# Performance work log

Measured on AMD Instinct MI355X. Metric: run time of the kernel, lower is better.

## Reference

```python
import jax, jax.numpy as jnp
import numpy as np

B, T, C, H = 2, 2048, 1024, 16
HD = C // H  # head_size = 64
EPS = 1e-5


def setup_inputs() -> dict:
    key = jax.random.key(0)
    ks = jax.random.split(key, 12)
    s = lambda fan_in: 1.0 / np.sqrt(fan_in)
    return {
        "x": jax.random.normal(ks[0], (B, T, C), jnp.float32),
        # attention projections, stored [in, out] so y = x @ W
        "Wq": jax.random.normal(ks[1], (C, C), jnp.float32) * s(C),
        "Wk": jax.random.normal(ks[2], (C, C), jnp.float32) * s(C),
        "Wv": jax.random.normal(ks[3], (C, C), jnp.float32) * s(C),
        "Wo": jax.random.normal(ks[4], (C, C), jnp.float32) * s(C),
        "bo": jnp.zeros((C,), jnp.float32),
        "ln1_g": jnp.ones((C,), jnp.float32),
        "ln1_b": jnp.zeros((C,), jnp.float32),
        "ln2_g": jnp.ones((C,), jnp.float32),
        "ln2_b": jnp.zeros((C,), jnp.float32),
        "W1": jax.random.normal(ks[5], (C, 4 * C), jnp.float32) * s(C),
        "b1": jnp.zeros((4 * C,), jnp.float32),
        "W2": jax.random.normal(ks[6], (4 * C, C), jnp.float32) * s(4 * C),
        "b2": jnp.zeros((C,), jnp.float32),
    }


def _layernorm(x, g, b):
    mu = jnp.mean(x, axis=-1, keepdims=True)
    var = jnp.mean(jnp.square(x - mu), axis=-1, keepdims=True)
    return (x - mu) * jax.lax.rsqrt(var + EPS) * g + b


def reference(x, Wq, Wk, Wv, Wo, bo, ln1_g, ln1_b, ln2_g, ln2_b, W1, b1, W2, b2):
    # Dropout layers are inference no-ops (eval mode).
    Bz, Tz, Cz = x.shape
    h = _layernorm(x, ln1_g, ln1_b)
    # fused multi-head projections (equivalent to per-head Linears concatenated)
    q = (h @ Wq).reshape(Bz, Tz, H, HD)
    k = (h @ Wk).reshape(Bz, Tz, H, HD)
    v = (h @ Wv).reshape(Bz, Tz, H, HD)
    scores = jnp.einsum("bqhd,bkhd->bhqk", q, k) / np.sqrt(HD).astype(np.float32)
    causal = jnp.tril(jnp.ones((Tz, Tz), bool))
    scores = jnp.where(causal, scores, -jnp.inf)
    attn = jax.nn.softmax(scores, axis=-1)
    out = jnp.einsum("bhqk,bkhd->bqhd", attn, v).reshape(Bz, Tz, Cz)
    x = x + out @ Wo + bo
    h2 = _layernorm(x, ln2_g, ln2_b)
    ff = jax.nn.relu(h2 @ W1 + b1) @ W2 + b2
    return x + ff
```

## Files before the change

### kernel.cpp

```cpp
#include <hip/hip_runtime.h>
#include <hip/hip_bf16.h>
#include <stdint.h>

#define B_  2
#define T_  2048
#define C_  1024
#define H_  16
#define HD_ 64
#define M_  4096
#define FF_ 4096

typedef unsigned short ushort_t;
typedef __bf16 bf16x8 __attribute__((ext_vector_type(8)));
typedef float  f32x4  __attribute__((ext_vector_type(4)));
typedef float  f32x16 __attribute__((ext_vector_type(16)));
typedef unsigned int u32x2 __attribute__((ext_vector_type(2)));
typedef unsigned int u32x4 __attribute__((ext_vector_type(4)));

#define C2_ 0.1803368801111204f

__device__ inline ushort_t f2bf(float f) {
  uint32_t u = __builtin_bit_cast(uint32_t, f);
  u += 0x7fffu + ((u >> 16) & 1u);
  return (ushort_t)(u >> 16);
}
__device__ inline uint32_t pk2(float lo, float hi) {
  return (uint32_t)f2bf(lo) | ((uint32_t)f2bf(hi) << 16);
}

__device__ inline void gload_lds16(const void* g, void* l) {
  __builtin_amdgcn_global_load_lds(
      (const __attribute__((address_space(1))) uint32_t*)g,
      (__attribute__((address_space(3))) uint32_t*)l, 16, 0, 0);
}

__device__ inline int qswz(int row, int byte_in_row) {
  return row * 128 + (byte_in_row ^ ((row & 7) << 4));
}

__global__ __launch_bounds__(256) void lnorm_kernel(
    const float* __restrict__ x, const float* __restrict__ g,
    const float* __restrict__ b, ushort_t* __restrict__ o) {
  int row = blockIdx.x;
  int tid = threadIdx.x;
  const float4* xr = (const float4*)(x + (size_t)row * C_);
  float4 xv = xr[tid];
  float s  = xv.x + xv.y + xv.z + xv.w;
  float s2 = xv.x*xv.x + xv.y*xv.y + xv.z*xv.z + xv.w*xv.w;
#pragma unroll
  for (int off = 32; off; off >>= 1) {
    s  += __shfl_down(s,  off);
    s2 += __shfl_down(s2, off);
  }
  __shared__ float rs[4], rq[4];
  int wid = tid >> 6;
  if ((tid & 63) == 0) { rs[wid] = s; rq[wid] = s2; }
  __syncthreads();
  float tot  = rs[0] + rs[1] + rs[2] + rs[3];
  float tot2 = rq[0] + rq[1] + rq[2] + rq[3];
  float mu   = tot * (1.0f / C_);
  float var  = tot2 * (1.0f / C_) - mu * mu;
  float rstd = rsqrtf(var + 1e-5f);
  float4 gv = ((const float4*)g)[tid];
  float4 bv = ((const float4*)b)[tid];
  float y0 = (xv.x - mu) * rstd * gv.x + bv.x;
  float y1 = (xv.y - mu) * rstd * gv.y + bv.y;
  float y2 = (xv.z - mu) * rstd * gv.z + bv.z;
  float y3 = (xv.w - mu) * rstd * gv.w + bv.w;
  uint2 pk;
  pk.x = (uint32_t)f2bf(y0) | ((uint32_t)f2bf(y1) << 16);
  pk.y = (uint32_t)f2bf(y2) | ((uint32_t)f2bf(y3) << 16);
  *(uint2*)(o + (size_t)row * C_ + tid * 4) = pk;
}

__global__ __launch_bounds__(256) void tcast_kernel(
    const float* __restrict__ W, ushort_t* __restrict__ Wt, int K, int N) {
  __shared__ float t[32][33];
  int bn = blockIdx.x, bk = blockIdx.y;
  int tx = threadIdx.x & 31, ty = threadIdx.x >> 5;
#pragma unroll
  for (int i = 0; i < 4; ++i)
    t[ty + i*8][tx] = W[(size_t)(bk*32 + ty + i*8) * N + bn*32 + tx];
  __syncthreads();
#pragma unroll
  for (int i = 0; i < 4; ++i)
    Wt[(size_t)(bn*32 + ty + i*8) * K + bk*32 + tx] = f2bf(t[tx][ty + i*8]);
}

__global__ __launch_bounds__(256) void vtrans_kernel(
    const ushort_t* __restrict__ qkv, ushort_t* __restrict__ vt) {
  __shared__ ushort_t t[32][33];
  int tt = blockIdx.x;
  int cc = blockIdx.y;
  int bb = blockIdx.z;
  int tx = threadIdx.x & 31, ty = threadIdx.x >> 5;
#pragma unroll
  for (int i = 0; i < 4; ++i)
    t[ty + i*8][tx] = qkv[(size_t)(bb*T_ + tt*32 + ty + i*8)*3072 + 2048 + cc*32 + tx];
  __syncthreads();
  int crow = threadIdx.x >> 4;
  int ucol = threadIdx.x & 15;
#pragma unroll
  for (int i = 0; i < 2; ++i) {
    int c = crow + i*16;
    uint32_t vlo = t[ucol*2][c], vhi = t[ucol*2 + 1][c];
    *(uint32_t*)&vt[(size_t)(bb*1024 + cc*32 + c)*T_ + tt*32 + ucol*2] =
        vlo | (vhi << 16);
  }
}

template<int BN, int BIAS, int RELU, int RESID, int OUTBF16>
__global__ __launch_bounds__(256) void gemm_kernel(
    const ushort_t* __restrict__ A, const ushort_t* __restrict__ Bt,
    const float* __restrict__ bias, const float* __restrict__ resid,
    void* __restrict__ outp, int M, int N, int K) {
  constexpr int NFR = BN / 32;
  __shared__ __align__(16) ushort_t As[2][128*32];
  __shared__ __align__(16) ushort_t Bs[2][BN*32];
  int bn = blockIdx.x, bm = blockIdx.y;
  int tid = threadIdx.x;
  int lane = tid & 63, wid = tid >> 6;
  int wr = (wid >> 1) * 64, wc = (wid & 1) * (BN / 2);
  int r = lane & 15, g = lane >> 4;
  int srow = tid >> 2, scc = (tid & 3) * 8;
  f32x4 acc[4][NFR] = {};
  int nk = K >> 5;

  const ushort_t* Abase = A  + (size_t)(bm*128) * K;
  const ushort_t* Bbase = Bt + (size_t)(bn*BN) * K;

#define STAGE_(bi, kt_)                                                        \
  do {                                                                         \
    gload_lds16(Abase + (size_t)srow * K + (kt_)*32 + scc, &As[bi][tid*8]);    \
    gload_lds16(Abase + (size_t)(srow + 64) * K + (kt_)*32 + scc,              \
                &As[bi][(tid + 256)*8]);                                       \
    gload_lds16(Bbase + (size_t)srow * K + (kt_)*32 + scc, &Bs[bi][tid*8]);    \
    if (BN == 128)                                                             \
      gload_lds16(Bbase + (size_t)(srow + 64) * K + (kt_)*32 + scc,            \
                  &Bs[bi][(tid + 256)*8]);                                     \
  } while (0)

  STAGE_(0, 0);
  __syncthreads();
  int buf = 0;
  for (int kt = 0; kt < nk; ++kt) {
    if (kt + 1 < nk) STAGE_(buf ^ 1, kt + 1);
    bf16x8 af[4], bfv[NFR];
#pragma unroll
    for (int m = 0; m < 4; ++m)
      af[m] = *(const bf16x8*)&As[buf][(wr + m*16 + r)*32 + g*8];
#pragma unroll
    for (int n = 0; n < NFR; ++n)
      bfv[n] = *(const bf16x8*)&Bs[buf][(wc + n*16 + r)*32 + g*8];
#pragma unroll
    for (int m = 0; m < 4; ++m)
#pragma unroll
      for (int n = 0; n < NFR; ++n)
        acc[m][n] = __builtin_amdgcn_mfma_f32_16x16x32_bf16(
            af[m], bfv[n], acc[m][n], 0, 0, 0);
    __syncthreads();
    buf ^= 1;
  }
#undef STAGE_

#pragma unroll
  for (int m = 0; m < 4; ++m)
#pragma unroll
    for (int n = 0; n < NFR; ++n)
#pragma unroll
      for (int e = 0; e < 4; ++e) {
        int row = bm*128 + wr + m*16 + g*4 + e;
        int col = bn*BN + wc + n*16 + r;
        float v = acc[m][n][e];
        if (BIAS)  v += bias[col];
        if (RESID) v += resid[(size_t)row * N + col];
        if (RELU)  v = fmaxf(v, 0.0f);
        if (OUTBF16) ((ushort_t*)outp)[(size_t)row * N + col] = f2bf(v);
        else         ((float*)outp)[(size_t)row * N + col]    = v;
      }
}

__global__ __launch_bounds__(256) void attn_kernel(
    const ushort_t* __restrict__ q, const ushort_t* __restrict__ k,
    const ushort_t* __restrict__ vt, ushort_t* __restrict__ o, int ldq) {
  int bid = blockIdx.x;
  int qbb = 15 - (bid & 15);
  int hh = (bid >> 4) & 15;
  int bb = bid >> 8;
  __shared__ __align__(16) ushort_t Ks[64*64];
  __shared__ __align__(16) ushort_t Vts[64*64];
  int tid = threadIdx.x, lane = tid & 63, w = tid >> 6;
  int qi = lane & 31, hi = lane >> 5;
  int qrow0 = qbb*128 + w*32;
  int qg = qrow0 + qi;
  int lt = 2*qbb + (w >> 1);
  int nkv = 2*qbb + 2;

  const ushort_t* qbase = q + ((size_t)(bb*T_ + qg))*ldq + hh*64;
  bf16x8 qv[4];
#pragma unroll
  for (int c = 0; c < 4; ++c)
    qv[c] = *(const bf16x8*)(qbase + c*16 + hi*8);

  const ushort_t* kbase = k  + ((size_t)bb*T_)*ldq + hh*64;
  const ushort_t* vbase = vt + ((size_t)(bb*1024 + hh*64))*T_;

  int r0s = tid >> 3;
  int s0  = ((tid & 7) ^ (r0s & 7)) * 8;

  f32x16 O0 = {}, O1 = {};
  float mrun = -1e30f, lrun = 0.f;

  for (int kt = 0; kt < nkv; ++kt) {
    gload_lds16(kbase + ((size_t)(kt*64 + r0s))*ldq + s0,      &Ks[tid*8]);
    gload_lds16(kbase + ((size_t)(kt*64 + r0s + 32))*ldq + s0, &Ks[(tid+256)*8]);
    gload_lds16(vbase + (size_t)r0s*T_ + kt*64 + s0,           &Vts[tid*8]);
    gload_lds16(vbase + (size_t)(r0s+32)*T_ + kt*64 + s0,      &Vts[(tid+256)*8]);
    __syncthreads();
    if (kt <= lt) {
      f32x16 a0 = {}, a1 = {};
#pragma unroll
      for (int c = 0; c < 4; ++c) {
        bf16x8 k0 = *(const bf16x8*)((char*)Ks + qswz(qi,      c*32 + hi*16));
        bf16x8 k1 = *(const bf16x8*)((char*)Ks + qswz(32 + qi, c*32 + hi*16));
        a0 = __builtin_amdgcn_mfma_f32_32x32x16_bf16(k0, qv[c], a0, 0, 0, 0);
        a1 = __builtin_amdgcn_mfma_f32_32x32x16_bf16(k1, qv[c], a1, 0, 0, 0);
      }
      if (kt == lt) {
        int kof = kt*64 + 4*hi;
#pragma unroll
        for (int rg = 0; rg < 16; ++rg) {
          int kp = kof + (rg & 3) + 8*(rg >> 2);
          if (kp > qg)      a0[rg] = -1e30f;
          if (kp + 32 > qg) a1[rg] = -1e30f;
        }
      }
      float tm = -1e30f;
#pragma unroll
      for (int rg = 0; rg < 16; ++rg) tm = fmaxf(tm, fmaxf(a0[rg], a1[rg]));
      tm = fmaxf(tm, __shfl_xor(tm, 32));
      float mnew = fmaxf(mrun, tm);
      float sf = exp2f((mrun - mnew) * C2_);
      mrun = mnew;
      float mc = mnew * C2_;
#pragma unroll
      for (int rg = 0; rg < 16; ++rg) {
        a0[rg] = exp2f(a0[rg]*C2_ - mc);
        a1[rg] = exp2f(a1[rg]*C2_ - mc);
      }
      float rs = 0.f;
#pragma unroll
      for (int rg = 0; rg < 16; ++rg) rs += a0[rg] + a1[rg];
      rs += __shfl_xor(rs, 32);
      lrun = lrun*sf + rs;
#pragma unroll
      for (int rg = 0; rg < 16; ++rg) { O0[rg] *= sf; O1[rg] *= sf; }
      bf16x8 pf[4];
#pragma unroll
      for (int kb = 0; kb < 2; ++kb)
#pragma unroll
        for (int jj = 0; jj < 2; ++jj) {
          int rb = jj*8;
          float v0 = kb ? a1[rb+0] : a0[rb+0], v1 = kb ? a1[rb+1] : a0[rb+1];
          float v2 = kb ? a1[rb+2] : a0[rb+2], v3 = kb ? a1[rb+3] : a0[rb+3];
          float v4 = kb ? a1[rb+4] : a0[rb+4], v5 = kb ? a1[rb+5] : a0[rb+5];
          float v6 = kb ? a1[rb+6] : a0[rb+6], v7 = kb ? a1[rb+7] : a0[rb+7];
          uint32_t d0 = pk2(v0, v1), d1 = pk2(v2, v3);
          uint32_t e0 = pk2(v4, v5), e1 = pk2(v6, v7);
          uint32_t pd0 = __shfl_xor(d0, 32), pd1 = __shfl_xor(d1, 32);
          uint32_t pe0 = __shfl_xor(e0, 32), pe1 = __shfl_xor(e1, 32);
          u32x4 fw;
          fw[0] = hi ? pe0 : d0;
          fw[1] = hi ? pe1 : d1;
          fw[2] = hi ? e0  : pd0;
          fw[3] = hi ? e1  : pd1;
          pf[kb*2 + jj] = __builtin_bit_cast(bf16x8, fw);
        }
#pragma unroll
      for (int kk = 0; kk < 4; ++kk) {
        bf16x8 vv0 = *(const bf16x8*)((char*)Vts + qswz(qi,      kk*32 + hi*16));
        bf16x8 vv1 = *(const bf16x8*)((char*)Vts + qswz(32 + qi, kk*32 + hi*16));
        O0 = __builtin_amdgcn_mfma_f32_32x32x16_bf16(vv0, pf[kk], O0, 0, 0, 0);
        O1 = __builtin_amdgcn_mfma_f32_32x32x16_bf16(vv1, pf[kk], O1, 0, 0, 0);
      }
    }
    __syncthreads();
  }
  float inv = 1.0f / lrun;
  ushort_t* ob = o + ((size_t)(bb*T_ + qg))*C_ + hh*64;
#pragma unroll
  for (int tq = 0; tq < 4; ++tq) {
    u32x2 st0, st1;
    st0[0] = pk2(O0[4*tq+0]*inv, O0[4*tq+1]*inv);
    st0[1] = pk2(O0[4*tq+2]*inv, O0[4*tq+3]*inv);
    st1[0] = pk2(O1[4*tq+0]*inv, O1[4*tq+1]*inv);
    st1[1] = pk2(O1[4*tq+2]*inv, O1[4*tq+3]*inv);
    *(u32x2*)(ob + 8*tq + 4*hi)      = st0;
    *(u32x2*)(ob + 32 + 8*tq + 4*hi) = st1;
  }
}

extern "C" void kernel_launch(void* const* d_in, const int* in_sizes, int n_in,
                              void* d_out, int out_size, void* d_ws, size_t ws_size,
                              hipStream_t stream) {
  const float* x    = (const float*)d_in[0];
  const float* Wq   = (const float*)d_in[1];
  const float* Wk   = (const float*)d_in[2];
  const float* Wv   = (const float*)d_in[3];
  const float* Wo   = (const float*)d_in[4];
  const float* bo   = (const float*)d_in[5];
  const float* ln1g = (const float*)d_in[6];
  const float* ln1b = (const float*)d_in[7];
  const float* ln2g = (const float*)d_in[8];
  const float* ln2b = (const float*)d_in[9];
  const float* W1   = (const float*)d_in[10];
  const float* b1   = (const float*)d_in[11];
  const float* W2   = (const float*)d_in[12];
  const float* b2   = (const float*)d_in[13];

  char* ws = (char*)d_ws;
  ushort_t* h    = (ushort_t*)(ws + ((size_t)0  << 20));
  ushort_t* vt   = (ushort_t*)(ws + ((size_t)0  << 20));
  ushort_t* qkv  = (ushort_t*)(ws + ((size_t)8  << 20));
  ushort_t* ff   = (ushort_t*)(ws + ((size_t)0  << 20));
  ushort_t* attn = (ushort_t*)(ws + ((size_t)32 << 20));
  float*    x2   = (float*)   (ws + ((size_t)40 << 20));
  ushort_t* h2   = (ushort_t*)(ws + ((size_t)56 << 20));
  ushort_t* wqt  = (ushort_t*)(ws + ((size_t)64 << 20));
  ushort_t* wkt  = (ushort_t*)(ws + ((size_t)66 << 20));
  ushort_t* wvt  = (ushort_t*)(ws + ((size_t)68 << 20));
  ushort_t* wot  = (ushort_t*)(ws + ((size_t)70 << 20));
  ushort_t* w1t  = (ushort_t*)(ws + ((size_t)72 << 20));
  ushort_t* w2t  = (ushort_t*)(ws + ((size_t)80 << 20));
  float* out = (float*)d_out;

  tcast_kernel<<<dim3(32, 32),  256, 0, stream>>>(Wq, wqt, 1024, 1024);
  tcast_kernel<<<dim3(32, 32),  256, 0, stream>>>(Wk, wkt, 1024, 1024);
  tcast_kernel<<<dim3(32, 32),  256, 0, stream>>>(Wv, wvt, 1024, 1024);
  tcast_kernel<<<dim3(32, 32),  256, 0, stream>>>(Wo, wot, 1024, 1024);
  tcast_kernel<<<dim3(128, 32), 256, 0, stream>>>(W1, w1t, 1024, 4096);
  tcast_kernel<<<dim3(32, 128), 256, 0, stream>>>(W2, w2t, 4096, 1024);

  lnorm_kernel<<<M_, 256, 0, stream>>>(x, ln1g, ln1b, h);

  gemm_kernel<128,0,0,0,1><<<dim3(24, 32), 256, 0, stream>>>(h, wqt, nullptr, nullptr, qkv, M_, 3*C_, C_);

  vtrans_kernel<<<dim3(64, 32, 2), 256, 0, stream>>>(qkv, vt);

  attn_kernel<<<512, 256, 0, stream>>>(qkv, qkv + C_, vt, attn, 3*C_);

  gemm_kernel<64,1,0,1,0><<<dim3(16, 32), 256, 0, stream>>>(attn, wot, bo, x, x2, M_, C_, C_);

  lnorm_kernel<<<M_, 256, 0, stream>>>(x2, ln2g, ln2b, h2);

  gemm_kernel<128,1,1,0,1><<<dim3(32, 32), 256, 0, stream>>>(h2, w1t, b1, nullptr, ff, M_, FF_, C_);

  gemm_kernel<64,1,0,1,0><<<dim3(16, 32), 256, 0, stream>>>(ff, w2t, b2, x2, out, M_, C_, FF_);
}
```

Baseline: 421.8 us.

## Double-buffer K/V tiles in attention and remap blocks across XCDs

The attention kernel now keeps two LDS buffers for K and V^T and issues the load for the next tile before computing on the current one, with one barrier per iteration. The goal is to overlap global-to-LDS transfer with MFMA work. The block index mapping also changes: the low three bits pick the head so each XCD handles a fixed set of heads, and query-block order is reversed for the second batch to balance causal work. LDS use doubles, which may reduce occupancy, and correctness relies on the async LDS loads finishing before the next barrier.

```diff
diff --git a/kernel.cpp b/kernel.cpp
--- a/kernel.cpp
+++ b/kernel.cpp
@@ -184,11 +184,13 @@
     const ushort_t* __restrict__ q, const ushort_t* __restrict__ k,
     const ushort_t* __restrict__ vt, ushort_t* __restrict__ o, int ldq) {
   int bid = blockIdx.x;
-  int qbb = 15 - (bid & 15);
-  int hh = (bid >> 4) & 15;
-  int bb = bid >> 8;
-  __shared__ __align__(16) ushort_t Ks[64*64];
-  __shared__ __align__(16) ushort_t Vts[64*64];
+  int xcd = bid & 7, kk_ = bid >> 3;
+  int q4 = kk_ & 15, rest = kk_ >> 4;
+  int hh = xcd + 8*(rest & 1);
+  int bb = rest >> 1;
+  int qbb = bb ? (15 - q4) : q4;
+  __shared__ __align__(16) ushort_t Ks[2][64*64];
+  __shared__ __align__(16) ushort_t Vts[2][64*64];
   int tid = threadIdx.x, lane = tid & 63, w = tid >> 6;
   int qi = lane & 31, hi = lane >> 5;
   int qrow0 = qbb*128 + w*32;
@@ -211,18 +213,27 @@
   f32x16 O0 = {}, O1 = {};
   float mrun = -1e30f, lrun = 0.f;
 
+#define AST_(bi, kt_)                                                          \
+  do {                                                                         \
+    gload_lds16(kbase + ((size_t)((kt_)*64 + r0s))*ldq + s0, &Ks[bi][tid*8]);  \
+    gload_lds16(kbase + ((size_t)((kt_)*64 + r0s + 32))*ldq + s0,              \
+                &Ks[bi][(tid+256)*8]);                                         \
+    gload_lds16(vbase + (size_t)r0s*T_ + (kt_)*64 + s0, &Vts[bi][tid*8]);      \
+    gload_lds16(vbase + (size_t)(r0s+32)*T_ + (kt_)*64 + s0,                   \
+                &Vts[bi][(tid+256)*8]);                                        \
+  } while (0)
+
+  AST_(0, 0);
+  __syncthreads();
+  int buf = 0;
   for (int kt = 0; kt < nkv; ++kt) {
-    gload_lds16(kbase + ((size_t)(kt*64 + r0s))*ldq + s0,      &Ks[tid*8]);
-    gload_lds16(kbase + ((size_t)(kt*64 + r0s + 32))*ldq + s0, &Ks[(tid+256)*8]);
-    gload_lds16(vbase + (size_t)r0s*T_ + kt*64 + s0,           &Vts[tid*8]);
-    gload_lds16(vbase + (size_t)(r0s+32)*T_ + kt*64 + s0,      &Vts[(tid+256)*8]);
-    __syncthreads();
+    if (kt + 1 < nkv) AST_(buf ^ 1, kt + 1);
     if (kt <= lt) {
       f32x16 a0 = {}, a1 = {};
 #pragma unroll
       for (int c = 0; c < 4; ++c) {
-        bf16x8 k0 = *(const bf16x8*)((char*)Ks + qswz(qi,      c*32 + hi*16));
-        bf16x8 k1 = *(const bf16x8*)((char*)Ks + qswz(32 + qi, c*32 + hi*16));
+        bf16x8 k0 = *(const bf16x8*)((char*)&Ks[buf][0] + qswz(qi,      c*32 + hi*16));
+        bf16x8 k1 = *(const bf16x8*)((char*)&Ks[buf][0] + qswz(32 + qi, c*32 + hi*16));
         a0 = __builtin_amdgcn_mfma_f32_32x32x16_bf16(k0, qv[c], a0, 0, 0, 0);
         a1 = __builtin_amdgcn_mfma_f32_32x32x16_bf16(k1, qv[c], a1, 0, 0, 0);
       }
@@ -278,14 +289,16 @@
         }
 #pragma unroll
       for (int kk = 0; kk < 4; ++kk) {
-        bf16x8 vv0 = *(const bf16x8*)((char*)Vts + qswz(qi,      kk*32 + hi*16));
-        bf16x8 vv1 = *(const bf16x8*)((char*)Vts + qswz(32 + qi, kk*32 + hi*16));
+        bf16x8 vv0 = *(const bf16x8*)((char*)&Vts[buf][0] + qswz(qi,      kk*32 + hi*16));
+        bf16x8 vv1 = *(const bf16x8*)((char*)&Vts[buf][0] + qswz(32 + qi, kk*32 + hi*16));
         O0 = __builtin_amdgcn_mfma_f32_32x32x16_bf16(vv0, pf[kk], O0, 0, 0, 0);
         O1 = __builtin_amdgcn_mfma_f32_32x32x16_bf16(vv1, pf[kk], O1, 0, 0, 0);
       }
     }
     __syncthreads();
-  }
+    buf ^= 1;
+  }
+#undef AST_
   float inv = 1.0f / lrun;
   ushort_t* ob = o + ((size_t)(bb*T_ + qg))*C_ + hh*64;
 #pragma unroll
```

Measured after the change: 401.7 us. 1.05x faster.
